# Optimization experiments

Measured on AMD Instinct MI355X. Metric: run time of the kernel, lower is better.

## Reference

```python
import jax, jax.numpy as jnp
import numpy as np

V_TH = 1.0

def spike_fn(x):
    # Heaviside spike (surrogate gradient only matters for bwd)
    return (x > 0).astype(x.dtype)

def setup_inputs() -> dict:
    key = jax.random.key(0)
    ks = jax.random.split(key, 7)
    B, T, I = 256, 512, 512
    H, NB, O = 1024, 4, 128
    HB = H // NB
    x = jax.random.normal(ks[0], (B, T, I), dtype=jnp.float32)
    v0 = jax.random.uniform(ks[1], (B, H), dtype=jnp.float32)  # torch.rand init
    W_branch = jax.random.normal(ks[2], (NB, I, HB), dtype=jnp.float32) * (1.0 / np.sqrt(I))
    tau_n = jax.random.uniform(ks[3], (NB, HB), minval=2.0, maxval=6.0, dtype=jnp.float32)
    tau_m = jax.random.uniform(ks[4], (H,), minval=0.0, maxval=4.0, dtype=jnp.float32)
    W_out = jax.random.normal(ks[5], (H, O), dtype=jnp.float32) * (1.0 / np.sqrt(H))
    b_out = jnp.zeros((O,), dtype=jnp.float32)
    return {"x": x, "v0": v0, "W_branch": W_branch, "tau_n": tau_n,
            "tau_m": tau_m, "W_out": W_out, "b_out": b_out}

def reference(x, v0, W_branch, tau_n, tau_m, W_out, b_out):
    B, T, I = x.shape
    NB, _, HB = W_branch.shape
    H = NB * HB
    beta = jax.nn.sigmoid(tau_n)[:, None, :]   # (NB, 1, HB)
    alpha = jax.nn.sigmoid(tau_m)              # (H,)
    xt = jnp.transpose(x, (1, 0, 2))           # (T, B, I)
    mask = (jnp.arange(T) >= T // 2).astype(x.dtype)  # integrate 2nd half only

    def step(carry, inp):
        d, v, s, acc = carry
        x_t, m = inp
        branch_in = jnp.einsum('bi,nio->nbo', x_t, W_branch)  # (NB, B, HB)
        d = beta * d + (1.0 - beta) * branch_in
        total = jnp.transpose(d, (1, 0, 2)).reshape(B, H)      # cat branches dim=1
        v = alpha * v + (1.0 - alpha) * total - V_TH * s
        s = spike_fn(v - V_TH)
        acc = acc + s * m
        return (d, v, s, acc), None

    d0 = jnp.zeros((NB, B, HB), dtype=x.dtype)
    s0 = jnp.zeros((B, H), dtype=x.dtype)
    acc0 = jnp.zeros((B, H), dtype=x.dtype)
    (d, v, s, acc), _ = jax.lax.scan(step, (d0, v0, s0, acc0), (xt, mask))
    return acc @ W_out + b_out
```

## Files before the change

kernel.cpp:

```cpp
#include <hip/hip_runtime.h>
#include <hip/hip_bf16.h>

#define BSZ 256
#define TT  512
#define II  512
#define HH  1024
#define OO  128
#define BH  262144

#define BM 128
#define BN 128
#define BK 32
#define LDA 40

typedef short bfrag8 __attribute__((ext_vector_type(8)));
typedef float f32x4  __attribute__((ext_vector_type(4)));
typedef short s16x4  __attribute__((ext_vector_type(4)));

__device__ __forceinline__ unsigned short f2bf(float f) {
    union { float f; unsigned int u; } c; c.f = f;
    unsigned int u = c.u;
    unsigned int r = u + 0x7fffu + ((u >> 16) & 1u);
    return (unsigned short)(r >> 16);
}
__device__ __forceinline__ float bf2f(unsigned short h) {
    union { unsigned int u; float f; } c; c.u = ((unsigned int)h) << 16;
    return c.f;
}

__device__ __forceinline__ void split2(float f0, float f1, s16x4* hi_dst, s16x4* lo_dst, int off) {
    __hip_bfloat162 h2 = __float22bfloat162_rn(make_float2(f0, f1));
    float r0 = f0 - __bfloat162float(h2.x);
    float r1 = f1 - __bfloat162float(h2.y);
    __hip_bfloat162 l2 = __float22bfloat162_rn(make_float2(r0, r1));
    union { __hip_bfloat162 b; int i; } ch, cl;
    ch.b = h2; cl.b = l2;
    ((int*)hi_dst)[off] = ch.i;
    ((int*)lo_dst)[off] = cl.i;
}

__global__ __launch_bounds__(256) void setup_k(const float* __restrict__ Wb,
                                               const float* __restrict__ v0,
                                               unsigned short* __restrict__ Whi,
                                               unsigned short* __restrict__ Wlo,
                                               float* __restrict__ dS, float* __restrict__ vS,
                                               float* __restrict__ sS, float* __restrict__ aS) {
    int idx = blockIdx.x * 256 + threadIdx.x;
    int n = idx >> 17;
    int rem = idx & 131071;
    int i = rem >> 8;
    int o = rem & 255;
    int h = (n << 8) + o;
    float w = Wb[idx];
    unsigned short hi = f2bf(w);
    float fh = bf2f(hi);
    unsigned short lo = f2bf(w - fh);
    Whi[(size_t)h * II + i] = hi;
    Wlo[(size_t)h * II + i] = lo;
    if (idx < BH) {
        dS[idx] = 0.0f; vS[idx] = v0[idx]; sS[idx] = 0.0f; aS[idx] = 0.0f;
    }
}

__global__ __launch_bounds__(256, 2) void gemm_split(
    const float* __restrict__ X, const unsigned short* __restrict__ Whi,
    const unsigned short* __restrict__ Wlo, float* __restrict__ U,
    int t0, int lgTc)
{
    __shared__ __align__(16) short Ah[BM * LDA];
    __shared__ __align__(16) short Al[BM * LDA];
    __shared__ __align__(16) short Bh[BN * LDA];
    __shared__ __align__(16) short Bl[BN * LDA];

    const int n_tile = blockIdx.x;
    const int m_tile = blockIdx.y;
    const int m0 = m_tile * BM;
    const int h0 = n_tile * BN;
    const int tid = threadIdx.x;
    const int lane = tid & 63;
    const int wave = tid >> 6;
    const int wm = wave & 1, wn = wave >> 1;
    const int l16 = lane & 15, q = lane >> 4;

    f32x4 acc[4][4];
#pragma unroll
    for (int i = 0; i < 4; ++i)
#pragma unroll
        for (int j = 0; j < 4; ++j)
#pragma unroll
            for (int r = 0; r < 4; ++r) acc[i][j][r] = 0.0f;

    const int fr = tid & 7;
    const int r0 = tid >> 3;
    const int cB = tid & 3;
    const int nB = tid >> 2;

    for (int k0 = 0; k0 < II; k0 += BK) {
#pragma unroll
        for (int p = 0; p < 4; ++p) {
            int r = r0 + p * 32;
            int m = m0 + r;
            int bb = m >> lgTc;
            int tl = m - (bb << lgTc);
            const float4* src = (const float4*)(X + ((size_t)(bb * TT + t0 + tl)) * II + k0 + fr * 4);
            float4 val = *src;
            s16x4 hi4, lo4;
            split2(val.x, val.y, &hi4, &lo4, 0);
            split2(val.z, val.w, &hi4, &lo4, 1);
            *(s16x4*)&Ah[r * LDA + fr * 4] = hi4;
            *(s16x4*)&Al[r * LDA + fr * 4] = lo4;
        }
#pragma unroll
        for (int p = 0; p < 2; ++p) {
            int n = nB + p * 64;
            *(uint4*)&Bh[n * LDA + cB * 8] = *(const uint4*)(Whi + (size_t)(h0 + n) * II + k0 + cB * 8);
            *(uint4*)&Bl[n * LDA + cB * 8] = *(const uint4*)(Wlo + (size_t)(h0 + n) * II + k0 + cB * 8);
        }
        __syncthreads();

        bfrag8 ah[4], al[4], bh[4], bl[4];
#pragma unroll
        for (int i = 0; i < 4; ++i) {
            int ra = (wm * 64 + i * 16 + l16) * LDA + q * 8;
            ah[i] = *(const bfrag8*)&Ah[ra];
            al[i] = *(const bfrag8*)&Al[ra];
            int rb = (wn * 64 + i * 16 + l16) * LDA + q * 8;
            bh[i] = *(const bfrag8*)&Bh[rb];
            bl[i] = *(const bfrag8*)&Bl[rb];
        }
#pragma unroll
        for (int im = 0; im < 4; ++im)
#pragma unroll
            for (int in = 0; in < 4; ++in) {
                f32x4 c = acc[im][in];
                c = __builtin_amdgcn_mfma_f32_16x16x32_bf16(ah[im], bh[in], c, 0, 0, 0);
                c = __builtin_amdgcn_mfma_f32_16x16x32_bf16(ah[im], bl[in], c, 0, 0, 0);
                c = __builtin_amdgcn_mfma_f32_16x16x32_bf16(al[im], bh[in], c, 0, 0, 0);
                acc[im][in] = c;
            }
        __syncthreads();
    }

#pragma unroll
    for (int im = 0; im < 4; ++im) {
        int rowb = wm * 64 + im * 16 + q * 4;
#pragma unroll
        for (int r = 0; r < 4; ++r) {
            int m = m0 + rowb + r;
            int bb = m >> lgTc;
            int tl = m - (bb << lgTc);
            size_t base = ((size_t)tl * BSZ + bb) * HH + h0 + wn * 64 + l16;
#pragma unroll
            for (int in = 0; in < 4; ++in)
                U[base + in * 16] = acc[im][in][r];
        }
    }
}

__global__ __launch_bounds__(256) void scan_chunk(const float* __restrict__ U,
    const float* __restrict__ tau_n, const float* __restrict__ tau_m,
    float* __restrict__ dS, float* __restrict__ vS,
    float* __restrict__ sS, float* __restrict__ aS, int t0, int Tc)
{
    int idx = blockIdx.x * 256 + threadIdx.x;
    int h = idx & (HH - 1);
    float beta  = 1.0f / (1.0f + __expf(-tau_n[h]));
    float alpha = 1.0f / (1.0f + __expf(-tau_m[h]));
    float ob = 1.0f - beta, oa = 1.0f - alpha;
    float dd = dS[idx], vv = vS[idx], ss = sS[idx], aa = aS[idx];
    const float* Up = U + idx;

    float u[16];
#pragma unroll
    for (int j = 0; j < 16; ++j) u[j] = Up[(size_t)j << 18];

    int tg = 0;
    for (; tg + 16 < Tc; tg += 16) {
#pragma unroll
        for (int j = 0; j < 16; ++j) {
            float uu = u[j];
            u[j] = Up[(size_t)(tg + 16 + j) << 18];
            float msk = ((t0 + tg + j) >= (TT / 2)) ? 1.0f : 0.0f;
            dd = beta * dd + ob * uu;
            vv = alpha * vv + oa * dd - ss;
            ss = (vv > 1.0f) ? 1.0f : 0.0f;
            aa += msk * ss;
        }
    }
#pragma unroll
    for (int j = 0; j < 16; ++j) {
        float uu = u[j];
        float msk = ((t0 + tg + j) >= (TT / 2)) ? 1.0f : 0.0f;
        dd = beta * dd + ob * uu;
        vv = alpha * vv + oa * dd - ss;
        ss = (vv > 1.0f) ? 1.0f : 0.0f;
        aa += msk * ss;
    }
    dS[idx] = dd; vS[idx] = vv; sS[idx] = ss; aS[idx] = aa;
}

__global__ __launch_bounds__(256) void out_gemm(const float* __restrict__ acc,
    const float* __restrict__ Wout, const float* __restrict__ bout,
    float* __restrict__ out)
{
    __shared__ float a_s[HH];
    __shared__ float partial[OO];
    int b = blockIdx.x;
    int o = threadIdx.x & (OO - 1);
    int half = threadIdx.x >> 7;
    for (int i = threadIdx.x; i < HH; i += 256) a_s[i] = acc[b * HH + i];
    __syncthreads();
    float sum = half ? 0.0f : bout[o];
    const float* Wp = Wout + (size_t)half * 512 * OO + o;
    const float* ap = a_s + half * 512;
#pragma unroll 8
    for (int h = 0; h < 512; ++h) sum = fmaf(ap[h], Wp[(size_t)h * OO], sum);
    if (half) partial[o] = sum;
    __syncthreads();
    if (!half) out[b * OO + o] = sum + partial[o];
}

extern "C" void kernel_launch(void* const* d_in, const int* in_sizes, int n_in,
                              void* d_out, int out_size, void* d_ws, size_t ws_size,
                              hipStream_t stream) {
    const float* x     = (const float*)d_in[0];
    const float* v0    = (const float*)d_in[1];
    const float* Wb    = (const float*)d_in[2];
    const float* tau_n = (const float*)d_in[3];
    const float* tau_m = (const float*)d_in[4];
    const float* Wout  = (const float*)d_in[5];
    const float* bout  = (const float*)d_in[6];
    float* out = (float*)d_out;

    char* ws = (char*)d_ws;
    unsigned short* Whi = (unsigned short*)(ws);
    unsigned short* Wlo = (unsigned short*)(ws + (1ll << 20));
    float* dS = (float*)(ws + (2ll << 20));
    float* vS = (float*)(ws + (3ll << 20));
    float* sS = (float*)(ws + (4ll << 20));
    float* aS = (float*)(ws + (5ll << 20));
    float* U  = (float*)(ws + (6ll << 20));

    long long avail = (long long)ws_size - (6ll << 20);
    int Tc = 512;
    while (Tc > 16 && (long long)Tc * (1ll << 20) > avail) Tc >>= 1;
    int lgTc = 31 - __builtin_clz((unsigned)Tc);

    setup_k<<<2048, 256, 0, stream>>>(Wb, v0, Whi, Wlo, dS, vS, sS, aS);

    for (int t0 = 0; t0 < TT; t0 += Tc) {
        dim3 grid(HH / BN, (BSZ * Tc) / BM);
        gemm_split<<<grid, 256, 0, stream>>>(x, Whi, Wlo, U, t0, lgTc);
        scan_chunk<<<BH / 256, 256, 0, stream>>>(U, tau_n, tau_m, dS, vS, sS, aS, t0, Tc);
    }
    out_gemm<<<BSZ, 256, 0, stream>>>(aS, Wout, bout, out);
}
```

Measured before the change: 876.3 us.

## Rewrite split-bf16 GEMM with async LDS loads, double buffering, 256x256 tiles

Replaces the 128x128 split-bf16 GEMM with a 512-thread, 256x256-tile kernel. Tiles are staged by global_load_lds into double-buffered, XOR-swizzled shared memory, and fp32 X is split into hi/lo bf16 at fragment-load time from LDS. It adds MFMA priority hints, a grid remap for L2 locality, and drops the workspace-based time chunking so the whole sequence runs in one GEMM and one scan launch. The risks are 128KB of LDS per block and the assumption that the workspace can hold the full U buffer.

```diff
diff --git a/kernel.cpp b/kernel.cpp
--- a/kernel.cpp
+++ b/kernel.cpp
@@ -8,14 +8,8 @@
 #define OO  128
 #define BH  262144
 
-#define BM 128
-#define BN 128
-#define BK 32
-#define LDA 40
-
 typedef short bfrag8 __attribute__((ext_vector_type(8)));
 typedef float f32x4  __attribute__((ext_vector_type(4)));
-typedef short s16x4  __attribute__((ext_vector_type(4)));
 
 __device__ __forceinline__ unsigned short f2bf(float f) {
     union { float f; unsigned int u; } c; c.f = f;
@@ -28,15 +22,23 @@
     return c.f;
 }
 
-__device__ __forceinline__ void split2(float f0, float f1, s16x4* hi_dst, s16x4* lo_dst, int off) {
+__device__ __forceinline__ void pack2(float f0, float f1, int& hi, int& lo) {
     __hip_bfloat162 h2 = __float22bfloat162_rn(make_float2(f0, f1));
     float r0 = f0 - __bfloat162float(h2.x);
     float r1 = f1 - __bfloat162float(h2.y);
     __hip_bfloat162 l2 = __float22bfloat162_rn(make_float2(r0, r1));
     union { __hip_bfloat162 b; int i; } ch, cl;
     ch.b = h2; cl.b = l2;
-    ((int*)hi_dst)[off] = ch.i;
-    ((int*)lo_dst)[off] = cl.i;
+    hi = ch.i; lo = cl.i;
+}
+
+__device__ __forceinline__ void split8(f32x4 a, f32x4 b, bfrag8& hi, bfrag8& lo) {
+    union { bfrag8 v; int i[4]; } H, L;
+    pack2(a.x, a.y, H.i[0], L.i[0]);
+    pack2(a.z, a.w, H.i[1], L.i[1]);
+    pack2(b.x, b.y, H.i[2], L.i[2]);
+    pack2(b.z, b.w, H.i[3], L.i[3]);
+    hi = H.v; lo = L.v;
 }
 
 __global__ __launch_bounds__(256) void setup_k(const float* __restrict__ Wb,
@@ -62,97 +64,150 @@
     }
 }
 
-__global__ __launch_bounds__(256, 2) void gemm_split(
-    const float* __restrict__ X, const unsigned short* __restrict__ Whi,
-    const unsigned short* __restrict__ Wlo, float* __restrict__ U,
-    int t0, int lgTc)
+#define GLL16(G, Lp) __builtin_amdgcn_global_load_lds(                         \
+    (const __attribute__((address_space(1))) void*)(G),                        \
+    (__attribute__((address_space(3))) void*)(Lp), 16, 0, 0)
+
+#define BAR() do { asm volatile("" ::: "memory");                              \
+                   __builtin_amdgcn_s_barrier();                               \
+                   asm volatile("" ::: "memory"); } while (0)
+
+#define STAGE(K0, BUFB) do {                                                   \
+    _Pragma("unroll") for (int j_ = 0; j_ < 4; ++j_) {                         \
+        int w8_ = (j_ << 3) + wv;                                              \
+        GLL16(gA + (K0) + ((size_t)w8_ << 12), smem + (BUFB) + (w8_ << 10));   \
+        GLL16(gB + (K0) + ((size_t)w8_ << 12), smem + (BUFB) + 32768 + (w8_ << 10)); \
+    } } while (0)
+
+#define LOADA2(F, BUFB, H0, L0, H1, L1) do {                                   \
+    const char* p_ = smem + (BUFB) + aRow + ((F) << 11);                       \
+    f32x4 x0_ = *(const f32x4*)(p_ + aO0);                                     \
+    f32x4 x1_ = *(const f32x4*)(p_ + aO1);                                     \
+    f32x4 x2_ = *(const f32x4*)(p_ + 2048 + aO0);                              \
+    f32x4 x3_ = *(const f32x4*)(p_ + 2048 + aO1);                              \
+    split8(x0_, x1_, H0, L0);                                                  \
+    split8(x2_, x3_, H1, L1);                                                  \
+} while (0)
+
+#define LOADB(BUFB) do {                                                       \
+    const char* p_ = smem + (BUFB) + bRow;                                     \
+    _Pragma("unroll") for (int g_ = 0; g_ < 4; ++g_) {                         \
+        bh[g_] = *(const bfrag8*)(p_ + (g_ << 11) + bO0);                      \
+        bl[g_] = *(const bfrag8*)(p_ + (g_ << 11) + bO1);                      \
+    } } while (0)
+
+#define MFMA3(AH, AL, BHG, BLG, C) do {                                        \
+    C = __builtin_amdgcn_mfma_f32_16x16x32_bf16(AH, BHG, C, 0, 0, 0);          \
+    C = __builtin_amdgcn_mfma_f32_16x16x32_bf16(AH, BLG, C, 0, 0, 0);          \
+    C = __builtin_amdgcn_mfma_f32_16x16x32_bf16(AL, BHG, C, 0, 0, 0);          \
+} while (0)
+
+#define MM2(F, H0, L0, H1, L1) do {                                            \
+    __builtin_amdgcn_s_setprio(1);                                             \
+    _Pragma("unroll") for (int g_ = 0; g_ < 4; ++g_) {                         \
+        MFMA3(H0, L0, bh[g_], bl[g_], acc[F][g_]);                             \
+        MFMA3(H1, L1, bh[g_], bl[g_], acc[(F) + 1][g_]);                       \
+    }                                                                          \
+    __builtin_amdgcn_s_setprio(0);                                             \
+} while (0)
+
+__global__ __launch_bounds__(512, 2) void gemm8(const float* __restrict__ X,
+    const unsigned short* __restrict__ Whi, const unsigned short* __restrict__ Wlo,
+    float* __restrict__ U)
 {
-    __shared__ __align__(16) short Ah[BM * LDA];
-    __shared__ __align__(16) short Al[BM * LDA];
-    __shared__ __align__(16) short Bh[BN * LDA];
-    __shared__ __align__(16) short Bl[BN * LDA];
-
-    const int n_tile = blockIdx.x;
-    const int m_tile = blockIdx.y;
-    const int m0 = m_tile * BM;
-    const int h0 = n_tile * BN;
+    extern __shared__ char smem[];
+
+    const int P = blockIdx.x;
+    const int L = ((P & 7) << 8) | (P >> 3);
+    const int m0 = (L >> 2) << 8;
+    const int h0 = (L & 3) << 8;
+
     const int tid = threadIdx.x;
     const int lane = tid & 63;
-    const int wave = tid >> 6;
-    const int wm = wave & 1, wn = wave >> 1;
-    const int l16 = lane & 15, q = lane >> 4;
-
-    f32x4 acc[4][4];
-#pragma unroll
-    for (int i = 0; i < 4; ++i)
+    const int wv = tid >> 6;
+    const int l16 = lane & 15;
+    const int q = lane >> 4;
+    const int wm = wv >> 2, wn = wv & 3;
+
+    const int e = l16 & 7;
+    const int aRow = ((wm << 7) + l16) << 7;
+    const int aO0 = ((((q << 1)    ) ^ e) << 4);
+    const int aO1 = ((((q << 1) | 1) ^ e) << 4);
+    const int bRow = (((wn << 6) + l16) << 7) + 32768;
+    const int bO0 = (((q    ) ^ e) << 4);
+    const int bO1 = (((q + 4) ^ e) << 4);
+
+    const int rl = lane >> 3;
+    const int sp = (lane & 7) ^ (rl & 7);
+    const float* gA = X + ((size_t)(m0 + rl) << 9) + (sp << 2);
+    const unsigned short* gB = (sp < 4)
+        ? (Whi + ((size_t)(h0 + rl) << 9) + (sp << 3))
+        : (Wlo + ((size_t)(h0 + rl) << 9) + ((sp - 4) << 3));
+
+    f32x4 acc[8][4];
+#pragma unroll
+    for (int i = 0; i < 8; ++i)
 #pragma unroll
         for (int j = 0; j < 4; ++j)
 #pragma unroll
             for (int r = 0; r < 4; ++r) acc[i][j][r] = 0.0f;
 
-    const int fr = tid & 7;
-    const int r0 = tid >> 3;
-    const int cB = tid & 3;
-    const int nB = tid >> 2;
-
-    for (int k0 = 0; k0 < II; k0 += BK) {
-#pragma unroll
-        for (int p = 0; p < 4; ++p) {
-            int r = r0 + p * 32;
-            int m = m0 + r;
-            int bb = m >> lgTc;
-            int tl = m - (bb << lgTc);
-            const float4* src = (const float4*)(X + ((size_t)(bb * TT + t0 + tl)) * II + k0 + fr * 4);
-            float4 val = *src;
-            s16x4 hi4, lo4;
-            split2(val.x, val.y, &hi4, &lo4, 0);
-            split2(val.z, val.w, &hi4, &lo4, 1);
-            *(s16x4*)&Ah[r * LDA + fr * 4] = hi4;
-            *(s16x4*)&Al[r * LDA + fr * 4] = lo4;
-        }
-#pragma unroll
-        for (int p = 0; p < 2; ++p) {
-            int n = nB + p * 64;
-            *(uint4*)&Bh[n * LDA + cB * 8] = *(const uint4*)(Whi + (size_t)(h0 + n) * II + k0 + cB * 8);
-            *(uint4*)&Bl[n * LDA + cB * 8] = *(const uint4*)(Wlo + (size_t)(h0 + n) * II + k0 + cB * 8);
-        }
-        __syncthreads();
-
-        bfrag8 ah[4], al[4], bh[4], bl[4];
-#pragma unroll
-        for (int i = 0; i < 4; ++i) {
-            int ra = (wm * 64 + i * 16 + l16) * LDA + q * 8;
-            ah[i] = *(const bfrag8*)&Ah[ra];
-            al[i] = *(const bfrag8*)&Al[ra];
-            int rb = (wn * 64 + i * 16 + l16) * LDA + q * 8;
-            bh[i] = *(const bfrag8*)&Bh[rb];
-            bl[i] = *(const bfrag8*)&Bl[rb];
-        }
-#pragma unroll
-        for (int im = 0; im < 4; ++im)
-#pragma unroll
-            for (int in = 0; in < 4; ++in) {
-                f32x4 c = acc[im][in];
-                c = __builtin_amdgcn_mfma_f32_16x16x32_bf16(ah[im], bh[in], c, 0, 0, 0);
-                c = __builtin_amdgcn_mfma_f32_16x16x32_bf16(ah[im], bl[in], c, 0, 0, 0);
-                c = __builtin_amdgcn_mfma_f32_16x16x32_bf16(al[im], bh[in], c, 0, 0, 0);
-                acc[im][in] = c;
-            }
-        __syncthreads();
-    }
-
-#pragma unroll
-    for (int im = 0; im < 4; ++im) {
-        int rowb = wm * 64 + im * 16 + q * 4;
-#pragma unroll
-        for (int r = 0; r < 4; ++r) {
-            int m = m0 + rowb + r;
-            int bb = m >> lgTc;
-            int tl = m - (bb << lgTc);
-            size_t base = ((size_t)tl * BSZ + bb) * HH + h0 + wn * 64 + l16;
-#pragma unroll
-            for (int in = 0; in < 4; ++in)
-                U[base + in * 16] = acc[im][in][r];
+    bfrag8 a0h, a0l, a1h, a1l;
+    bfrag8 b0h, b0l, b1h, b1l;
+    bfrag8 bh[4], bl[4];
+
+    STAGE(0, 0);
+    STAGE(32, 65536);
+    asm volatile("s_waitcnt vmcnt(8)" ::: "memory");
+    __builtin_amdgcn_s_barrier();
+    asm volatile("" ::: "memory");
+    LOADA2(0, 0, a0h, a0l, a1h, a1l);
+
+#pragma unroll 1
+    for (int tt = 0; tt < 16; tt += 2) {
+        const int k2 = (tt << 5) + 64;
+        LOADB(0);
+        LOADA2(2, 0, b0h, b0l, b1h, b1l);
+        MM2(0, a0h, a0l, a1h, a1l);
+        BAR();
+        LOADA2(4, 0, a0h, a0l, a1h, a1l);
+        MM2(2, b0h, b0l, b1h, b1l);
+        BAR();
+        LOADA2(6, 0, b0h, b0l, b1h, b1l);
+        MM2(4, a0h, a0l, a1h, a1l);
+        asm volatile("s_waitcnt vmcnt(0) lgkmcnt(0)" ::: "memory");
+        BAR();
+        if (tt < 14) STAGE(k2, 0);
+        LOADA2(0, 65536, a0h, a0l, a1h, a1l);
+        MM2(6, b0h, b0l, b1h, b1l);
+        BAR();
+        LOADB(65536);
+        LOADA2(2, 65536, b0h, b0l, b1h, b1l);
+        MM2(0, a0h, a0l, a1h, a1l);
+        BAR();
+        LOADA2(4, 65536, a0h, a0l, a1h, a1l);
+        MM2(2, b0h, b0l, b1h, b1l);
+        BAR();
+        LOADA2(6, 65536, b0h, b0l, b1h, b1l);
+        MM2(4, a0h, a0l, a1h, a1l);
+        asm volatile("s_waitcnt vmcnt(0) lgkmcnt(0)" ::: "memory");
+        BAR();
+        if (tt < 13) STAGE(k2 + 32, 65536);
+        if (tt < 14) LOADA2(0, 0, a0h, a0l, a1h, a1l);
+        MM2(6, b0h, b0l, b1h, b1l);
+        BAR();
+    }
+
+#pragma unroll
+    for (int f = 0; f < 8; ++f) {
+        const int rb = m0 + (wm << 7) + (f << 4) + (q << 2);
+#pragma unroll
+        for (int rr = 0; rr < 4; ++rr) {
+            const int m = rb + rr;
+            const size_t base =
+                (((size_t)((m & 511) << 8) + (m >> 9)) << 10) + h0 + (wn << 6) + l16;
+#pragma unroll
+            for (int g = 0; g < 4; ++g) U[base + (g << 4)] = acc[f][g][rr];
         }
     }
 }
@@ -241,17 +296,11 @@
     float* aS = (float*)(ws + (5ll << 20));
     float* U  = (float*)(ws + (6ll << 20));
 
-    long long avail = (long long)ws_size - (6ll << 20);
-    int Tc = 512;
-    while (Tc > 16 && (long long)Tc * (1ll << 20) > avail) Tc >>= 1;
-    int lgTc = 31 - __builtin_clz((unsigned)Tc);
+    hipFuncSetAttribute((const void*)gemm8,
+                        hipFuncAttributeMaxDynamicSharedMemorySize, 131072);
 
     setup_k<<<2048, 256, 0, stream>>>(Wb, v0, Whi, Wlo, dS, vS, sS, aS);
-
-    for (int t0 = 0; t0 < TT; t0 += Tc) {
-        dim3 grid(HH / BN, (BSZ * Tc) / BM);
-        gemm_split<<<grid, 256, 0, stream>>>(x, Whi, Wlo, U, t0, lgTc);
-        scan_chunk<<<BH / 256, 256, 0, stream>>>(U, tau_n, tau_m, dS, vS, sS, aS, t0, Tc);
-    }
+    gemm8<<<2048, 512, 131072, stream>>>(x, Whi, Wlo, U);
+    scan_chunk<<<BH / 256, 256, 0, stream>>>(U, tau_n, tau_m, dS, vS, sS, aS, 0, TT);
     out_gemm<<<BSZ, 256, 0, stream>>>(aS, Wout, bout, out);
 }
```

After: 962.3 us. 9.8% more time.
